# Kernel tuning notes

Measured on AMD Instinct MI355X. Metric: run time of the kernel, lower is better.

Reference implementation:

```python
import jax, jax.numpy as jnp
import numpy as np

BITWIDTH = 4  # sqllm 4-bit packing: 8 codes per int32


def sqllm_dequant4(qweight, lut):
    # qweight: [num_int32s, N] int32 (stored packed); lut: [N, 16]
    qw = qweight.T  # [N, num_int32s]
    shifts = jnp.arange(8, dtype=jnp.int32) * 4  # [8]
    # extract 8 nibbles per int32 -> indices in [0, 16)
    idx = (qw[:, :, None] >> shifts[None, None, :]) & 15  # [N, num_int32s, 8]
    N = qw.shape[0]
    idx = idx.reshape(N, -1)  # [N, K] with K = num_int32s * 8
    return jnp.take_along_axis(lut, idx, axis=1)  # [N, K]


def setup_inputs() -> dict:
    key = jax.random.key(0)
    k1, k2, k3 = jax.random.split(key, 3)
    B, S, K, N = 4, 2048, 4096, 4096
    inp = {
        "input": jax.random.normal(k1, (B, S, K), dtype=jnp.float32),
        "qweight": jax.random.randint(k2, (K // 8, N), 0, 2147483647, dtype=jnp.int32),
        "lut": jax.random.normal(k3, (N, 16), dtype=jnp.float32),
    }
    return inp


def reference(input, qweight, lut):
    # sqllm_gemm: dequantize packed 4-bit weights via LUT gather, then input @ W.T
    weights = sqllm_dequant4(qweight, lut)  # [N, K]
    return jnp.einsum("bsk,nk->bsn", input, weights)  # [B, S, N]
```

## Files before the change

### kernel.cpp

```cpp
#include <hip/hip_runtime.h>
#include <hip/hip_bf16.h>


typedef __attribute__((ext_vector_type(4))) float  f32x4;
typedef __attribute__((ext_vector_type(4))) int    i32x4;
typedef __attribute__((ext_vector_type(8))) short  bf16x8;

__device__ __forceinline__ unsigned short f2bf(float f) {
    __hip_bfloat16 h = __float2bfloat16(f);
    return __builtin_bit_cast(unsigned short, h);
}

__device__ __forceinline__ void gload16(const unsigned short* g, unsigned short* l) {
    __builtin_amdgcn_global_load_lds(
        (const __attribute__((address_space(1))) unsigned int*)g,
        (__attribute__((address_space(3))) unsigned int*)l, 16, 0, 0);
}


__global__ void convA_kernel(const float* __restrict__ in, unsigned short* __restrict__ o, long n8) {
    long i = (long)blockIdx.x * blockDim.x + threadIdx.x;
    long stride = (long)gridDim.x * blockDim.x;
    const f32x4* in4 = reinterpret_cast<const f32x4*>(in);
    bf16x8* o8 = reinterpret_cast<bf16x8*>(o);
    for (; i < n8; i += stride) {
        f32x4 a = in4[2 * i];
        f32x4 b = in4[2 * i + 1];
        bf16x8 e;
#pragma unroll
        for (int x = 0; x < 4; ++x) {
            e[x]     = (short)f2bf(a[x]);
            e[4 + x] = (short)f2bf(b[x]);
        }
        o8[i] = e;
    }
}

__global__ void dequantW_kernel(const int* __restrict__ Q, const float* __restrict__ lut,
                                unsigned short* __restrict__ Wb, int N, long total) {
    long i = (long)blockIdx.x * blockDim.x + threadIdx.x;
    if (i >= total) return;
    unsigned int v = (unsigned int)Q[i];
    int n = (int)(i % N);
    const float* lp = lut + (long)n * 16;
    bf16x8 w;
#pragma unroll
    for (int p = 0; p < 8; ++p)
        w[p] = (short)f2bf(lp[(v >> (4 * p)) & 15]);
    reinterpret_cast<bf16x8*>(Wb)[i] = w;
}


#define VM8 asm volatile("s_waitcnt vmcnt(8)" ::: "memory")

#define MFMA4(MF, AF) \
    acc[MF][0] = __builtin_amdgcn_mfma_f32_16x16x32_bf16(AF, bv0, acc[MF][0], 0, 0, 0); \
    acc[MF][1] = __builtin_amdgcn_mfma_f32_16x16x32_bf16(AF, bv1, acc[MF][1], 0, 0, 0); \
    acc[MF][2] = __builtin_amdgcn_mfma_f32_16x16x32_bf16(AF, bv2, acc[MF][2], 0, 0, 0); \
    acc[MF][3] = __builtin_amdgcn_mfma_f32_16x16x32_bf16(AF, bv3, acc[MF][3], 0, 0, 0);

#define DO_PHASE(SA, SB, MH, STAGE, WAIT) do {                                  \
    bf16x8 av0 = *(const bf16x8*)((SA) + aoff + (MH * 4 + 0) * 512);            \
    bf16x8 av1 = *(const bf16x8*)((SA) + aoff + (MH * 4 + 1) * 512);            \
    bf16x8 av2 = *(const bf16x8*)((SA) + aoff + (MH * 4 + 2) * 512);            \
    bf16x8 av3 = *(const bf16x8*)((SA) + aoff + (MH * 4 + 3) * 512);            \
    bf16x8 bv0 = *(const bf16x8*)((SB) + boff + 0 * 128);                       \
    bf16x8 bv1 = *(const bf16x8*)((SB) + boff + 1 * 128);                       \
    bf16x8 bv2 = *(const bf16x8*)((SB) + boff + 2 * 128);                       \
    bf16x8 bv3 = *(const bf16x8*)((SB) + boff + 3 * 128);                       \
    STAGE;                                                                      \
    WAIT;                                                                       \
    __builtin_amdgcn_s_barrier();                                               \
    __builtin_amdgcn_s_setprio(1);                                              \
    MFMA4(MH * 4 + 0, av0)                                                      \
    MFMA4(MH * 4 + 1, av1)                                                      \
    MFMA4(MH * 4 + 2, av2)                                                      \
    MFMA4(MH * 4 + 3, av3)                                                      \
    __builtin_amdgcn_s_setprio(0);                                              \
    __builtin_amdgcn_s_barrier();                                               \
} while (0)

__global__ __launch_bounds__(512, 2)
void gemm8p(const unsigned short* __restrict__ Abf, const unsigned short* __restrict__ Wb,
            float* __restrict__ out, int M, int N, int K) {
    __shared__ __align__(16) unsigned short sA[4 * 8192];
    __shared__ __align__(16) unsigned short sB[4 * 8192];

    const int tid  = threadIdx.x;
    const int lane = tid & 63;
    const int wid  = tid >> 6;
    const int wr   = wid >> 2;
    const int wc   = wid & 3;
    const int r15  = lane & 15;
    const int hi   = lane >> 4;

    int nwg = gridDim.x, orig = blockIdx.x;
    int wg = ((nwg & 7) == 0) ? (orig & 7) * (nwg >> 3) + (orig >> 3) : orig;
    const int NBN = N / 256;
    const int m0 = (wg / NBN) * 256, n0 = (wg % NBN) * 256;

    const int KT = K / 64;

    const int aoff = (wr * 128 + r15) * 32 + ((hi ^ ((r15 >> 1) & 3)) << 3);
    const int boff = hi * 2048 + (wc * 64 + r15) * 8;

    auto stageA = [&](int tau, int kh, int slot) {
#pragma unroll
        for (int j = 0; j < 2; ++j) {
            int idx = j * 512 + tid;
            int m = idx >> 2, kc = idx & 3;
            const unsigned short* src = Abf + (size_t)(m0 + m) * K + tau * 64 + kh * 32
                                        + ((kc ^ ((m >> 1) & 3)) << 3);
            gload16(src, sA + slot * 8192 + j * 4096 + wid * 512);
        }
    };
    auto stageB = [&](int tau, int kh, int slot) {
#pragma unroll
        for (int j = 0; j < 2; ++j) {
            int idx = j * 512 + tid;
            int kc = idx >> 8, n = idx & 255;
            const unsigned short* src = Wb + ((size_t)(tau * 8 + kh * 4 + kc) * N + n0 + n) * 8;
            gload16(src, sB + slot * 8192 + j * 4096 + wid * 512);
        }
    };

    f32x4 acc[8][4] = {};

    stageA(0, 0, 0); stageB(0, 0, 0);
    stageA(0, 1, 1); stageB(0, 1, 1);
    stageA(1, 0, 2); stageB(1, 0, 2);
    VM8;
    __builtin_amdgcn_s_barrier();

    const unsigned short* A0 = sA + 0 * 8192; const unsigned short* B0 = sB + 0 * 8192;
    const unsigned short* A1 = sA + 1 * 8192; const unsigned short* B1 = sB + 1 * 8192;
    const unsigned short* A2 = sA + 2 * 8192; const unsigned short* B2 = sB + 2 * 8192;
    const unsigned short* A3 = sA + 3 * 8192; const unsigned short* B3 = sB + 3 * 8192;

    for (int t = 0; t < KT; t += 2) {
        const int ta = t + 1;
        const int tb = (t + 2 == KT) ? 0 : t + 2;
        const int tc = (t + 3 >= KT) ? (t + 3 - KT) : t + 3;
        DO_PHASE(A0, B0, 0, stageA(ta, 1, 3), );
        DO_PHASE(A0, B0, 1, stageB(ta, 1, 3), VM8);
        DO_PHASE(A1, B1, 0, stageA(tb, 0, 0), );
        DO_PHASE(A1, B1, 1, stageB(tb, 0, 0), VM8);
        DO_PHASE(A2, B2, 0, stageA(tb, 1, 1), );
        DO_PHASE(A2, B2, 1, stageB(tb, 1, 1), VM8);
        DO_PHASE(A3, B3, 0, stageA(tc, 0, 2), );
        DO_PHASE(A3, B3, 1, stageB(tc, 0, 2), VM8);
    }

    asm volatile("s_waitcnt vmcnt(0)" ::: "memory");

#pragma unroll
    for (int mf = 0; mf < 8; ++mf) {
        const int mrow = m0 + wr * 128 + mf * 16 + hi * 4;
#pragma unroll
        for (int nf = 0; nf < 4; ++nf) {
            const int ncol = n0 + wc * 64 + nf * 16 + r15;
            float* po = out + (size_t)mrow * N + ncol;
#pragma unroll
            for (int r = 0; r < 4; ++r) po[(size_t)r * N] = acc[mf][nf][r];
        }
    }
}


#define FBM 128
#define FBN 128
#define FBK 64

__device__ __forceinline__ int fswz(int row, int kb) {
    return row * (FBK * 2) + (kb ^ ((row & 7) << 4));
}

__global__ __launch_bounds__(256, 2)
void sqllm_gemm_fused(const float* __restrict__ A, const int* __restrict__ Q,
                      const float* __restrict__ lut, float* __restrict__ out,
                      int M, int N, int K) {
    __shared__ __align__(16) char sA[FBM * FBK * 2];
    __shared__ __align__(16) char sB[FBN * FBK * 2];
    __shared__ float sLut[FBN * 17];

    const int tid  = threadIdx.x;
    const int lane = tid & 63;
    const int wid  = tid >> 6;
    const int wr   = wid >> 1;
    const int wc   = wid & 1;
    const int n0 = blockIdx.x * FBN;
    const int m0 = blockIdx.y * FBM;

    for (int i = tid; i < FBN * 16; i += 256) {
        int n = i >> 4, c = i & 15;
        sLut[n * 17 + c] = lut[(long)(n0 + n) * 16 + c];
    }
    __syncthreads();

    f32x4 acc[4][4] = {};
    const int nK = K / FBK;
    for (int kk = 0; kk < nK; ++kk) {
        {
            const int r = tid >> 1, h = tid & 1;
            const float* ap = A + (long)(m0 + r) * K + kk * FBK + h * 32;
            f32x4 v[8];
#pragma unroll
            for (int j = 0; j < 8; ++j) v[j] = reinterpret_cast<const f32x4*>(ap)[j];
            const int kr = tid >> 5, nq = (tid & 31) << 2;
            const int* qp = Q + (long)(kk * (FBK / 8) + kr) * N + n0 + nq;
            i32x4 q = *reinterpret_cast<const i32x4*>(qp);
#pragma unroll
            for (int j = 0; j < 4; ++j) {
                bf16x8 e;
#pragma unroll
                for (int x = 0; x < 4; ++x) {
                    e[x]     = (short)f2bf(v[2 * j][x]);
                    e[4 + x] = (short)f2bf(v[2 * j + 1][x]);
                }
                *reinterpret_cast<bf16x8*>(sA + fswz(r, h * 64 + j * 16)) = e;
            }
#pragma unroll
            for (int c = 0; c < 4; ++c) {
                const int n = nq + c;
                const float* lp = sLut + n * 17;
                unsigned int qq = (unsigned int)q[c];
                bf16x8 w;
#pragma unroll
                for (int p = 0; p < 8; ++p)
                    w[p] = (short)f2bf(lp[(qq >> (4 * p)) & 15]);
                *reinterpret_cast<bf16x8*>(sB + fswz(n, kr * 16)) = w;
            }
        }
        __syncthreads();
#pragma unroll
        for (int kh = 0; kh < 2; ++kh) {
            const int kb = kh * 64 + (lane >> 4) * 16;
            bf16x8 af[4], bfv[4];
#pragma unroll
            for (int i = 0; i < 4; ++i) {
                af[i]  = *reinterpret_cast<const bf16x8*>(sA + fswz(wr * 64 + i * 16 + (lane & 15), kb));
                bfv[i] = *reinterpret_cast<const bf16x8*>(sB + fswz(wc * 64 + i * 16 + (lane & 15), kb));
            }
#pragma unroll
            for (int i = 0; i < 4; ++i)
#pragma unroll
                for (int j = 0; j < 4; ++j)
                    acc[i][j] = __builtin_amdgcn_mfma_f32_16x16x32_bf16(af[i], bfv[j], acc[i][j], 0, 0, 0);
        }
        __syncthreads();
    }
    const int col = lane & 15;
    const int r4  = (lane >> 4) * 4;
#pragma unroll
    for (int i = 0; i < 4; ++i) {
        const int mrow = m0 + wr * 64 + i * 16 + r4;
#pragma unroll
        for (int j = 0; j < 4; ++j) {
            const int ncol = n0 + wc * 64 + j * 16 + col;
#pragma unroll
            for (int r = 0; r < 4; ++r)
                out[(long)(mrow + r) * N + ncol] = acc[i][j][r];
        }
    }
}

extern "C" void kernel_launch(void* const* d_in, const int* in_sizes, int n_in,
                              void* d_out, int out_size, void* d_ws, size_t ws_size,
                              hipStream_t stream) {
    const float* A   = (const float*)d_in[0];
    const int*   Q   = (const int*)d_in[1];
    const float* lut = (const float*)d_in[2];
    float* out = (float*)d_out;

    const long szA = in_sizes[0], szQ = in_sizes[1], szL = in_sizes[2];
    const int N = (int)(szL / 16);
    const int K = (int)(szQ * 8 / N);
    const int M = (int)(szA / K);

    const size_t needA = (size_t)M * K * 2;
    const size_t needW = (size_t)K * N * 2;

    const bool shape_ok = (M % 256 == 0) && (N % 256 == 0) && (K % 128 == 0);

    if (shape_ok && ws_size >= needA + needW) {
        unsigned short* Abf = (unsigned short*)d_ws;
        unsigned short* Wb  = (unsigned short*)((char*)d_ws + needA);
        const long n8 = (long)M * K / 8;
        convA_kernel<<<2048, 256, 0, stream>>>(A, Abf, n8);
        const long tq = (long)(K / 8) * N;
        dequantW_kernel<<<(int)((tq + 255) / 256), 256, 0, stream>>>(Q, lut, Wb, N, tq);
        dim3 grid((M / 256) * (N / 256));
        gemm8p<<<grid, 512, 0, stream>>>(Abf, Wb, out, M, N, K);
    } else {
        dim3 grid(N / FBN, M / FBM);
        sqllm_gemm_fused<<<grid, 256, 0, stream>>>(A, Q, lut, out, M, N, K);
    }
}
```

Baseline: 301.6 us.

## Merge GEMM half-phases into one phase per k-slab with combined A/B staging

```diff
diff --git a/kernel.cpp b/kernel.cpp
--- a/kernel.cpp
+++ b/kernel.cpp
@@ -51,35 +51,6 @@
 }
 
 
-#define VM8 asm volatile("s_waitcnt vmcnt(8)" ::: "memory")
-
-#define MFMA4(MF, AF) \
-    acc[MF][0] = __builtin_amdgcn_mfma_f32_16x16x32_bf16(AF, bv0, acc[MF][0], 0, 0, 0); \
-    acc[MF][1] = __builtin_amdgcn_mfma_f32_16x16x32_bf16(AF, bv1, acc[MF][1], 0, 0, 0); \
-    acc[MF][2] = __builtin_amdgcn_mfma_f32_16x16x32_bf16(AF, bv2, acc[MF][2], 0, 0, 0); \
-    acc[MF][3] = __builtin_amdgcn_mfma_f32_16x16x32_bf16(AF, bv3, acc[MF][3], 0, 0, 0);
-
-#define DO_PHASE(SA, SB, MH, STAGE, WAIT) do {                                  \
-    bf16x8 av0 = *(const bf16x8*)((SA) + aoff + (MH * 4 + 0) * 512);            \
-    bf16x8 av1 = *(const bf16x8*)((SA) + aoff + (MH * 4 + 1) * 512);            \
-    bf16x8 av2 = *(const bf16x8*)((SA) + aoff + (MH * 4 + 2) * 512);            \
-    bf16x8 av3 = *(const bf16x8*)((SA) + aoff + (MH * 4 + 3) * 512);            \
-    bf16x8 bv0 = *(const bf16x8*)((SB) + boff + 0 * 128);                       \
-    bf16x8 bv1 = *(const bf16x8*)((SB) + boff + 1 * 128);                       \
-    bf16x8 bv2 = *(const bf16x8*)((SB) + boff + 2 * 128);                       \
-    bf16x8 bv3 = *(const bf16x8*)((SB) + boff + 3 * 128);                       \
-    STAGE;                                                                      \
-    WAIT;                                                                       \
-    __builtin_amdgcn_s_barrier();                                               \
-    __builtin_amdgcn_s_setprio(1);                                              \
-    MFMA4(MH * 4 + 0, av0)                                                      \
-    MFMA4(MH * 4 + 1, av1)                                                      \
-    MFMA4(MH * 4 + 2, av2)                                                      \
-    MFMA4(MH * 4 + 3, av3)                                                      \
-    __builtin_amdgcn_s_setprio(0);                                              \
-    __builtin_amdgcn_s_barrier();                                               \
-} while (0)
-
 __global__ __launch_bounds__(512, 2)
 void gemm8p(const unsigned short* __restrict__ Abf, const unsigned short* __restrict__ Wb,
             float* __restrict__ out, int M, int N, int K) {
@@ -99,57 +70,61 @@
     const int NBN = N / 256;
     const int m0 = (wg / NBN) * 256, n0 = (wg % NBN) * 256;
 
-    const int KT = K / 64;
+    const int NH = K / 32;
 
     const int aoff = (wr * 128 + r15) * 32 + ((hi ^ ((r15 >> 1) & 3)) << 3);
     const int boff = hi * 2048 + (wc * 64 + r15) * 8;
 
-    auto stageA = [&](int tau, int kh, int slot) {
+    auto stage = [&](int S, int slot) {
 #pragma unroll
         for (int j = 0; j < 2; ++j) {
             int idx = j * 512 + tid;
             int m = idx >> 2, kc = idx & 3;
-            const unsigned short* src = Abf + (size_t)(m0 + m) * K + tau * 64 + kh * 32
-                                        + ((kc ^ ((m >> 1) & 3)) << 3);
-            gload16(src, sA + slot * 8192 + j * 4096 + wid * 512);
+            const unsigned short* srcA = Abf + (size_t)(m0 + m) * K + S * 32
+                                         + ((kc ^ ((m >> 1) & 3)) << 3);
+            gload16(srcA, sA + slot * 8192 + j * 4096 + wid * 512);
+            int kc2 = idx >> 8, n = idx & 255;
+            const unsigned short* srcB = Wb + ((size_t)(S * 4 + kc2) * N + n0 + n) * 8;
+            gload16(srcB, sB + slot * 8192 + j * 4096 + wid * 512);
         }
     };
-    auto stageB = [&](int tau, int kh, int slot) {
-#pragma unroll
-        for (int j = 0; j < 2; ++j) {
-            int idx = j * 512 + tid;
-            int kc = idx >> 8, n = idx & 255;
-            const unsigned short* src = Wb + ((size_t)(tau * 8 + kh * 4 + kc) * N + n0 + n) * 8;
-            gload16(src, sB + slot * 8192 + j * 4096 + wid * 512);
-        }
-    };
 
     f32x4 acc[8][4] = {};
 
-    stageA(0, 0, 0); stageB(0, 0, 0);
-    stageA(0, 1, 1); stageB(0, 1, 1);
-    stageA(1, 0, 2); stageB(1, 0, 2);
-    VM8;
+    stage(0, 0);
+    stage(1, 1);
+    stage(2, 2);
+    asm volatile("s_waitcnt vmcnt(8)" ::: "memory");
     __builtin_amdgcn_s_barrier();
 
-    const unsigned short* A0 = sA + 0 * 8192; const unsigned short* B0 = sB + 0 * 8192;
-    const unsigned short* A1 = sA + 1 * 8192; const unsigned short* B1 = sB + 1 * 8192;
-    const unsigned short* A2 = sA + 2 * 8192; const unsigned short* B2 = sB + 2 * 8192;
-    const unsigned short* A3 = sA + 3 * 8192; const unsigned short* B3 = sB + 3 * 8192;
-
-    for (int t = 0; t < KT; t += 2) {
-        const int ta = t + 1;
-        const int tb = (t + 2 == KT) ? 0 : t + 2;
-        const int tc = (t + 3 >= KT) ? (t + 3 - KT) : t + 3;
-        DO_PHASE(A0, B0, 0, stageA(ta, 1, 3), );
-        DO_PHASE(A0, B0, 1, stageB(ta, 1, 3), VM8);
-        DO_PHASE(A1, B1, 0, stageA(tb, 0, 0), );
-        DO_PHASE(A1, B1, 1, stageB(tb, 0, 0), VM8);
-        DO_PHASE(A2, B2, 0, stageA(tb, 1, 1), );
-        DO_PHASE(A2, B2, 1, stageB(tb, 1, 1), VM8);
-        DO_PHASE(A3, B3, 0, stageA(tc, 0, 2), );
-        DO_PHASE(A3, B3, 1, stageB(tc, 0, 2), VM8);
-    }
+#define PHASE(U) do {                                                             \
+    const unsigned short* SA = sA + (U) * 8192;                                   \
+    const unsigned short* SB = sB + (U) * 8192;                                   \
+    bf16x8 av[8], bv[4];                                                          \
+    _Pragma("unroll") for (int nf = 0; nf < 4; ++nf)                              \
+        bv[nf] = *(const bf16x8*)(SB + boff + nf * 128);                          \
+    _Pragma("unroll") for (int mf = 0; mf < 8; ++mf)                              \
+        av[mf] = *(const bf16x8*)(SA + aoff + mf * 512);                          \
+    int S = H + (U) + 3; if (S >= NH) S -= NH;                                    \
+    stage(S, ((U) + 3) & 3);                                                      \
+    asm volatile("s_waitcnt vmcnt(8)" ::: "memory");                              \
+    __builtin_amdgcn_s_barrier();                                                 \
+    __builtin_amdgcn_s_setprio(1);                                                \
+    _Pragma("unroll") for (int mf = 0; mf < 8; ++mf)                              \
+        _Pragma("unroll") for (int nf = 0; nf < 4; ++nf)                          \
+            acc[mf][nf] = __builtin_amdgcn_mfma_f32_16x16x32_bf16(                \
+                av[mf], bv[nf], acc[mf][nf], 0, 0, 0);                            \
+    __builtin_amdgcn_s_setprio(0);                                                \
+    __builtin_amdgcn_s_barrier();                                                 \
+} while (0)
+
+    for (int H = 0; H < NH; H += 4) {
+        PHASE(0);
+        PHASE(1);
+        PHASE(2);
+        PHASE(3);
+    }
+#undef PHASE
 
     asm volatile("s_waitcnt vmcnt(0)" ::: "memory");
 
```

After: 299.5 us. Within noise of the previous version (-0.7%).
